# Kernel optimization log

Hardware: AMD Instinct MI355X
Metric: run time of the kernel (lower is better)

Reference implementation:

```python
import jax, jax.numpy as jnp
import numpy as np

B, T, V = 32, 256, 32000

def setup_inputs() -> dict:
    key = jax.random.key(0)
    k1, k2, k3 = jax.random.split(key, 3)
    prediction = jax.random.normal(k1, (B, T, V), dtype=jnp.float32)
    groundtruth = jax.random.randint(k2, (B, T), 0, V, dtype=jnp.int64)
    lengths = jax.random.randint(k3, (B,), 0, T, dtype=jnp.int64)
    return {"prediction": prediction, "groundtruth": groundtruth, "lengths": lengths}

def reference(prediction, groundtruth, lengths):
    # Equivalent of: concat prediction[i][:lengths[i]-1] over i, then mean CE.
    # Implemented as masked cross-entropy: positions t < lengths[i]-1 are valid.
    Bv, Tv, Vv = prediction.shape
    tgt_len = lengths - 1                                   # [B]
    mask = jnp.arange(Tv)[None, :] < tgt_len[:, None]        # [B, T] bool
    logp = jax.nn.log_softmax(prediction, axis=-1)           # [B, T, V]
    nll = -jnp.take_along_axis(logp, groundtruth[..., None], axis=-1)[..., 0]  # [B, T]
    n_valid = jnp.maximum(jnp.sum(mask), 1)
    loss = jnp.sum(jnp.where(mask, nll, 0.0)) / n_valid.astype(prediction.dtype)
    return loss
```

## Files before the change

kernel.cpp:

```cpp
#include <hip/hip_runtime.h>
#include <math.h>

#define Bv 32
#define Tv 256
#define Vv 32000
#define NV4 (Vv / 4)

__global__ __launch_bounds__(256) void row_nll_kernel(const float* __restrict__ pred,
                                                      const int*   __restrict__ gt,
                                                      const int*   __restrict__ lens,
                                                      float*       __restrict__ row_nll) {
    const int r   = blockIdx.x;
    const int b   = r >> 8;
    const int t   = r & 255;
    const int tid = threadIdx.x;

    const int tgt_len = lens[b] - 1;
    if (t >= tgt_len) {
        if (tid == 0) row_nll[r] = 0.0f;
        return;
    }

    const float4* row = reinterpret_cast<const float4*>(pred + (size_t)r * Vv);

    float s = 0.0f;
    for (int i = tid; i < NV4; i += 256) {
        float4 v = row[i];
        s += __expf(v.x) + __expf(v.y) + __expf(v.z) + __expf(v.w);
    }

    __shared__ float red[4];
    const int wave = tid >> 6;
    const int lane = tid & 63;
    #pragma unroll
    for (int off = 32; off; off >>= 1) s += __shfl_xor(s, off);
    if (lane == 0) red[wave] = s;
    __syncthreads();
    if (tid == 0) {
        float ss = red[0] + red[1] + red[2] + red[3];
        float xg = pred[(size_t)r * Vv + gt[r]];
        row_nll[r] = logf(ss) - xg;
    }
}

__global__ __launch_bounds__(1024) void finalize_kernel(const float* __restrict__ row_nll,
                                                        const int*   __restrict__ lens,
                                                        float*       __restrict__ out) {
    const int tid = threadIdx.x;
    float s = 0.0f;
    for (int i = tid; i < Bv * Tv; i += 1024) s += row_nll[i];

    __shared__ float red[16];
    const int wave = tid >> 6;
    const int lane = tid & 63;
    #pragma unroll
    for (int off = 32; off; off >>= 1) s += __shfl_xor(s, off);
    if (lane == 0) red[wave] = s;
    __syncthreads();
    if (tid == 0) {
        float ss = 0.0f;
        #pragma unroll
        for (int w = 0; w < 16; ++w) ss += red[w];
        long long cnt = 0;
        for (int bb = 0; bb < Bv; ++bb) {
            int c = lens[bb] - 1;
            if (c > 0) cnt += c;
        }
        if (cnt < 1) cnt = 1;
        out[0] = ss / (float)cnt;
    }
}

extern "C" void kernel_launch(void* const* d_in, const int* in_sizes, int n_in,
                              void* d_out, int out_size, void* d_ws, size_t ws_size,
                              hipStream_t stream) {
    const float* pred = (const float*)d_in[0];
    const int*   gt   = (const int*)d_in[1];
    const int*   lens = (const int*)d_in[2];
    float*       out  = (float*)d_out;
    float*       row_nll = (float*)d_ws;

    row_nll_kernel<<<Bv * Tv, 256, 0, stream>>>(pred, gt, lens, row_nll);
    finalize_kernel<<<1, 1024, 0, stream>>>(row_nll, lens, out);
}
```

Baseline: 102.3 us.

## Split each row's exp-sum across two blocks with unrolled dual-accumulator loads

Each row's vocab is now split into two halves handled by separate blocks, which doubles the grid so more loads are in flight and load balance improves when many rows are masked. The inner loop is fully unrolled with two independent accumulators to raise memory-level parallelism. The finalize kernel now applies the mask, adds the two partial sums, takes the log and subtracts the gathered target logit. This costs an extra workspace array and more per-row work in the single-block finalize.

```diff
diff --git a/kernel.cpp b/kernel.cpp
--- a/kernel.cpp
+++ b/kernel.cpp
@@ -4,30 +4,47 @@
 #define Bv 32
 #define Tv 256
 #define Vv 32000
-#define NV4 (Vv / 4)
+#define HALF 16000
+#define NV4H 4000
 
-__global__ __launch_bounds__(256) void row_nll_kernel(const float* __restrict__ pred,
-                                                      const int*   __restrict__ gt,
-                                                      const int*   __restrict__ lens,
-                                                      float*       __restrict__ row_nll) {
-    const int r   = blockIdx.x;
+__device__ __forceinline__ float exp4(float4 v) {
+    return __expf(v.x) + __expf(v.y) + __expf(v.z) + __expf(v.w);
+}
+
+__global__ __launch_bounds__(256) void row_partial_kernel(const float* __restrict__ pred,
+                                                          const int*   __restrict__ gt,
+                                                          const int*   __restrict__ lens,
+                                                          float*       __restrict__ partial,
+                                                          float*       __restrict__ xg) {
+    const int bid = blockIdx.x;
+    const int r   = bid >> 1;
+    const int h   = bid & 1;
     const int b   = r >> 8;
     const int t   = r & 255;
     const int tid = threadIdx.x;
 
     const int tgt_len = lens[b] - 1;
-    if (t >= tgt_len) {
-        if (tid == 0) row_nll[r] = 0.0f;
-        return;
+    if (t >= tgt_len) return;
+
+    const float4* seg = reinterpret_cast<const float4*>(pred + (size_t)r * Vv + h * HALF);
+
+    float s0 = 0.0f, s1 = 0.0f;
+    #pragma unroll
+    for (int k = 0; k < 7; ++k) {
+        float4 a = seg[tid + 512 * k];
+        float4 c = seg[tid + 256 + 512 * k];
+        s0 += exp4(a);
+        s1 += exp4(c);
     }
-
-    const float4* row = reinterpret_cast<const float4*>(pred + (size_t)r * Vv);
-
-    float s = 0.0f;
-    for (int i = tid; i < NV4; i += 256) {
-        float4 v = row[i];
-        s += __expf(v.x) + __expf(v.y) + __expf(v.z) + __expf(v.w);
+    {
+        float4 a = seg[tid + 3584];
+        s0 += exp4(a);
     }
+    if (tid < 160) {
+        float4 a = seg[tid + 3840];
+        s1 += exp4(a);
+    }
+    float s = s0 + s1;
 
     __shared__ float red[4];
     const int wave = tid >> 6;
@@ -37,18 +54,23 @@
     if (lane == 0) red[wave] = s;
     __syncthreads();
     if (tid == 0) {
-        float ss = red[0] + red[1] + red[2] + red[3];
-        float xg = pred[(size_t)r * Vv + gt[r]];
-        row_nll[r] = logf(ss) - xg;
+        partial[bid] = red[0] + red[1] + red[2] + red[3];
+        if (h == 0) xg[r] = pred[(size_t)r * Vv + gt[r]];
     }
 }
 
-__global__ __launch_bounds__(1024) void finalize_kernel(const float* __restrict__ row_nll,
+__global__ __launch_bounds__(1024) void finalize_kernel(const float* __restrict__ partial,
+                                                        const float* __restrict__ xg,
                                                         const int*   __restrict__ lens,
                                                         float*       __restrict__ out) {
     const int tid = threadIdx.x;
     float s = 0.0f;
-    for (int i = tid; i < Bv * Tv; i += 1024) s += row_nll[i];
+    for (int r = tid; r < Bv * Tv; r += 1024) {
+        const int b = r >> 8;
+        const int t = r & 255;
+        if (t < lens[b] - 1)
+            s += logf(partial[2 * r] + partial[2 * r + 1]) - xg[r];
+    }
 
     __shared__ float red[16];
     const int wave = tid >> 6;
@@ -78,8 +100,9 @@
     const int*   gt   = (const int*)d_in[1];
     const int*   lens = (const int*)d_in[2];
     float*       out  = (float*)d_out;
-    float*       row_nll = (float*)d_ws;
+    float*       partial = (float*)d_ws;
+    float*       xg      = (float*)d_ws + 2 * Bv * Tv;
 
-    row_nll_kernel<<<Bv * Tv, 256, 0, stream>>>(pred, gt, lens, row_nll);
-    finalize_kernel<<<1, 1024, 0, stream>>>(row_nll, lens, out);
+    row_partial_kernel<<<2 * Bv * Tv, 256, 0, stream>>>(pred, gt, lens, partial, xg);
+    finalize_kernel<<<1, 1024, 0, stream>>>(partial, xg, lens, out);
 }
```

Result: faster. 94.08 us, median of 2 (-8.1%).
